# Optimization experiments

Hardware: AMD Instinct MI355X
Metric: run time of the kernel (lower is better)

## Reference

```python
import jax, jax.numpy as jnp
import numpy as np

B, N, C_IN, C_OUT, NUM_TYPES = 4, 4096, 128, 64, 5
TEMP = 1.0  # self.temp is undefined in the source; use 1.0


def setup_inputs() -> dict:
    key = jax.random.key(0)
    ks = jax.random.split(key, 9)
    bound_p = np.sqrt(6.0 / (C_IN + C_OUT))
    bound_k = np.sqrt(6.0 / (C_OUT + 1))
    return {
        "node_rep": jax.random.normal(ks[0], (B, N, C_IN), dtype=jnp.float32),
        "adj_matrix": jax.random.uniform(ks[1], (N, N), dtype=jnp.float32),
        "node_type": jax.random.randint(ks[2], (N,), 0, NUM_TYPES),
        "proj_W": jax.random.uniform(ks[3], (C_OUT, C_IN), minval=-bound_p, maxval=bound_p, dtype=jnp.float32),
        "proj_b": jnp.zeros((C_OUT,), dtype=jnp.float32),
        "k_W": jax.random.uniform(ks[4], (NUM_TYPES, C_OUT), minval=-bound_k, maxval=bound_k, dtype=jnp.float32),
        "k_b": jnp.zeros((NUM_TYPES,), dtype=jnp.float32),
        "v_W": jax.random.uniform(ks[5], (NUM_TYPES, C_OUT), minval=-bound_k, maxval=bound_k, dtype=jnp.float32),
        "v_b": jnp.zeros((NUM_TYPES,), dtype=jnp.float32),
    }


def reference(node_rep, adj_matrix, node_type, proj_W, proj_b, k_W, k_b, v_W, v_b):
    # projection: [B,N,c_in] -> [B,N,c_out]
    h = jnp.einsum('bnc,oc->bno', node_rep, proj_W) + proj_b
    # per-type scalar scores stacked: [B,N,num_types]
    ks = jnp.einsum('bno,to->bnt', h, k_W) + k_b
    vs = jnp.einsum('bno,to->bnt', h, v_W) + v_b
    # gather score of each node's own type -> [B,N,1]
    idx = jnp.broadcast_to(node_type[None, :, None], (h.shape[0], h.shape[1], 1))
    f1 = jnp.take_along_axis(ks, idx, axis=2)           # [B,N,1]
    f2 = jnp.take_along_axis(vs, idx, axis=2)           # [B,N,1]
    # pairwise logits masked/weighted by adjacency: [B,N,N]
    attn_logits = adj_matrix[None, :, :] * (f1 + jnp.swapaxes(f2, 1, 2))
    unnorm = jax.nn.sigmoid(attn_logits) - 0.5
    attn_probs = jax.nn.softmax(unnorm / TEMP, axis=1)  # softmax over dim 1, as in source
    # aggregate: [B,N,N] @ [B,N,c_out] -> [B,N,c_out]
    return jnp.matmul(attn_probs, h)
```

## Files before the change

### kernel.cpp

```cpp
#include <hip/hip_runtime.h>
#include <hip/hip_bf16.h>
#include <stdint.h>

#define NN   4096
#define BB   4
#define CIN  128
#define COUT 64

typedef __attribute__((ext_vector_type(4))) float f32x4;
typedef __attribute__((ext_vector_type(8))) short s16x8;
typedef __attribute__((ext_vector_type(4))) int   i32x4;

__device__ __forceinline__ float sig_exp(float u) {
    const float L = 1.4426950408889634f;
    float e0 = __builtin_amdgcn_exp2f(-u * L);
    float sg = __builtin_amdgcn_rcpf(1.0f + e0);
    return __builtin_amdgcn_exp2f(__builtin_fmaf(sg, L, -0.7213475204444817f));
}

__device__ __forceinline__ short f2bf(float x) {
    unsigned u = __builtin_bit_cast(unsigned, x);
    return (short)((u + 0x8000u) >> 16);
}

__global__ void k_zero(float* __restrict__ p, int n) {
    int i = blockIdx.x * blockDim.x + threadIdx.x;
    if (i < n) p[i] = 0.0f;
}

__global__ __launch_bounds__(256) void k_proj(
    const float* __restrict__ node_rep, const int* __restrict__ node_type,
    const float* __restrict__ pW, const float* __restrict__ pb,
    const float* __restrict__ kW, const float* __restrict__ kb,
    const float* __restrict__ vW, const float* __restrict__ vb,
    float* __restrict__ h, float* __restrict__ f1, float* __restrict__ f2)
{
    int row = blockIdx.x * 4 + (threadIdx.x >> 6);
    int o   = threadIdx.x & 63;
    int n   = row & (NN - 1);

    const f32x4* xr = (const f32x4*)(node_rep + (size_t)row * CIN);
    const f32x4* wr = (const f32x4*)(pW + (size_t)o * CIN);
    float acc = pb[o];
    #pragma unroll
    for (int c = 0; c < CIN / 4; ++c) {
        f32x4 x = xr[c], w = wr[c];
        acc = fmaf(x[0], w[0], acc);
        acc = fmaf(x[1], w[1], acc);
        acc = fmaf(x[2], w[2], acc);
        acc = fmaf(x[3], w[3], acc);
    }
    h[(size_t)row * COUT + o] = acc;

    int t = node_type[n];
    float s1 = acc * kW[t * COUT + o];
    float s2 = acc * vW[t * COUT + o];
    #pragma unroll
    for (int off = 32; off; off >>= 1) {
        s1 += __shfl_xor(s1, off, 64);
        s2 += __shfl_xor(s2, off, 64);
    }
    if (o == 0) { f1[row] = s1 + kb[t]; f2[row] = s2 + vb[t]; }
}

__global__ __launch_bounds__(256) void k_denom(
    const float* __restrict__ adj, const float* __restrict__ f1,
    const float* __restrict__ f2, float* __restrict__ denom)
{
    int j  = blockIdx.x * 256 + threadIdx.x;
    int i0 = blockIdx.y * 128;
    float f2r[BB], acc[BB];
    #pragma unroll
    for (int b = 0; b < BB; ++b) { f2r[b] = f2[b * NN + j]; acc[b] = 0.0f; }
    for (int ii = 0; ii < 128; ++ii) {
        int i = i0 + ii;
        float a = adj[(size_t)i * NN + j];
        #pragma unroll
        for (int b = 0; b < BB; ++b) {
            float u = a * (f1[b * NN + i] + f2r[b]);
            acc[b] += sig_exp(u);
        }
    }
    #pragma unroll
    for (int b = 0; b < BB; ++b) atomicAdd(&denom[b * NN + j], acc[b]);
}

__global__ __launch_bounds__(256) void k_hst(
    const float* __restrict__ h, const float* __restrict__ denom,
    unsigned short* __restrict__ hsT)
{
    int b  = blockIdx.y;
    int j0 = blockIdx.x * 64;
    __shared__ float tile[64][65];
    int cx = threadIdx.x & 63;
    int ry = threadIdx.x >> 6;
    #pragma unroll
    for (int k = 0; k < 16; ++k) {
        int jl = k * 4 + ry;
        float d = denom[b * NN + j0 + jl];
        tile[jl][cx] = h[((size_t)b * NN + j0 + jl) * COUT + cx] / d;
    }
    __syncthreads();
    #pragma unroll
    for (int k = 0; k < 16; ++k) {
        int cl = k * 4 + ry;
        hsT[((size_t)b * COUT + cl) * NN + j0 + cx] = (unsigned short)f2bf(tile[cx][cl]);
    }
}

__global__ __launch_bounds__(512) void k_out(
    const float* __restrict__ adj, const float* __restrict__ f1,
    const float* __restrict__ f2, const unsigned short* __restrict__ hsT,
    float* __restrict__ out)
{
    int i0   = blockIdx.x * 16;
    int tid  = threadIdx.x;
    int wid  = tid >> 6;
    int lane = tid & 63;
    int lrow = lane & 15;
    int lgrp = lane >> 4;

    const float* arow = adj + (size_t)(i0 + lrow) * NN;
    float f1v[BB];
    #pragma unroll
    for (int b = 0; b < BB; ++b) f1v[b] = f1[b * NN + i0 + lrow];

    f32x4 acc[BB][4];
    #pragma unroll
    for (int b = 0; b < BB; ++b)
        #pragma unroll
        for (int r = 0; r < 4; ++r) acc[b][r] = (f32x4){0.f, 0.f, 0.f, 0.f};

    int jbeg = wid * (NN / 8);
    for (int js = 0; js < NN / 8; js += 32) {
        int jk = jbeg + js + lgrp * 8;
        f32x4 a0 = *(const f32x4*)(arow + jk);
        f32x4 a1 = *(const f32x4*)(arow + jk + 4);

        #pragma unroll
        for (int b = 0; b < BB; ++b) {
            const float* f2b = f2 + b * NN;
            f32x4 s0 = *(const f32x4*)(f2b + jk);
            f32x4 s1 = *(const f32x4*)(f2b + jk + 4);

            float e[8];
            #pragma unroll
            for (int q = 0; q < 4; ++q) {
                e[q]     = sig_exp(a0[q] * (f1v[b] + s0[q]));
                e[q + 4] = sig_exp(a1[q] * (f1v[b] + s1[q]));
            }
            s16x8 af;
            #pragma unroll
            for (int q = 0; q < 8; ++q) af[q] = f2bf(e[q]);

            const unsigned short* hsb = hsT + (size_t)b * COUT * NN;
            s16x8 b0 = __builtin_bit_cast(s16x8, *(const i32x4*)(hsb + (size_t)(0  + lrow) * NN + jk));
            s16x8 b1 = __builtin_bit_cast(s16x8, *(const i32x4*)(hsb + (size_t)(16 + lrow) * NN + jk));
            s16x8 b2 = __builtin_bit_cast(s16x8, *(const i32x4*)(hsb + (size_t)(32 + lrow) * NN + jk));
            s16x8 b3 = __builtin_bit_cast(s16x8, *(const i32x4*)(hsb + (size_t)(48 + lrow) * NN + jk));

            acc[b][0] = __builtin_amdgcn_mfma_f32_16x16x32_bf16(af, b0, acc[b][0], 0, 0, 0);
            acc[b][1] = __builtin_amdgcn_mfma_f32_16x16x32_bf16(af, b1, acc[b][1], 0, 0, 0);
            acc[b][2] = __builtin_amdgcn_mfma_f32_16x16x32_bf16(af, b2, acc[b][2], 0, 0, 0);
            acc[b][3] = __builtin_amdgcn_mfma_f32_16x16x32_bf16(af, b3, acc[b][3], 0, 0, 0);
        }
    }

    __shared__ float red[8][16][64];
    #pragma unroll
    for (int b = 0; b < BB; ++b) {
        if (b) __syncthreads();
        #pragma unroll
        for (int r = 0; r < 4; ++r) {
            red[wid][lgrp * 4 + r][ 0 + lrow] = acc[b][0][r];
            red[wid][lgrp * 4 + r][16 + lrow] = acc[b][1][r];
            red[wid][lgrp * 4 + r][32 + lrow] = acc[b][2][r];
            red[wid][lgrp * 4 + r][48 + lrow] = acc[b][3][r];
        }
        __syncthreads();

        int e2 = tid * 2;
        int ii = e2 >> 6;
        int cc = e2 & 63;
        float sx = 0.f, sy = 0.f;
        #pragma unroll
        for (int w = 0; w < 8; ++w) {
            sx += red[w][ii][cc];
            sy += red[w][ii][cc + 1];
        }
        float* op = out + ((size_t)b * NN + i0 + ii) * COUT + cc;
        op[0] = sx; op[1] = sy;
    }
}

extern "C" void kernel_launch(void* const* d_in, const int* in_sizes, int n_in,
                              void* d_out, int out_size, void* d_ws, size_t ws_size,
                              hipStream_t stream)
{
    const float* node_rep = (const float*)d_in[0];
    const float* adj      = (const float*)d_in[1];
    const int*   ntype    = (const int*)  d_in[2];
    const float* pW       = (const float*)d_in[3];
    const float* pb       = (const float*)d_in[4];
    const float* kW       = (const float*)d_in[5];
    const float* kb       = (const float*)d_in[6];
    const float* vW       = (const float*)d_in[7];
    const float* vb       = (const float*)d_in[8];
    float* out = (float*)d_out;

    char* w = (char*)d_ws;
    float*          h     = (float*)(w);
    float*          f1    = (float*)(w + 4194304);
    float*          f2    = (float*)(w + 4259840);
    float*          denom = (float*)(w + 4325376);
    unsigned short* hsT   = (unsigned short*)(w + 4390912);

    k_zero <<<64, 256, 0, stream>>>(denom, BB * NN);
    k_proj <<<BB * NN / 4, 256, 0, stream>>>(node_rep, ntype, pW, pb, kW, kb, vW, vb, h, f1, f2);
    k_denom<<<dim3(NN / 256, 32), 256, 0, stream>>>(adj, f1, f2, denom);
    k_hst  <<<dim3(NN / 64, BB), 256, 0, stream>>>(h, denom, hsT);
    k_out  <<<dim3(NN / 16), 512, 0, stream>>>(adj, f1, f2, hsT, out);
}
```

Measured before the change: 334.0 us.

## Split denominator and output reductions into partial buffers with separate reduce kernels

The column-sum kernel now uses finer row tiles, so there are more blocks. It writes per-tile partial sums to a workspace, and a new reduce kernel turns them into reciprocal denominators. This replaces the atomics and the zeroing kernel. The output kernel splits the j dimension into four grid slices so more blocks are in flight, and a new kernel adds up the four partial outputs. The projection also uses four independent accumulators. The cost is extra workspace traffic, two extra launches, and a partial buffer of 16 MB for the output.

```diff
diff --git a/kernel.cpp b/kernel.cpp
--- a/kernel.cpp
+++ b/kernel.cpp
@@ -6,6 +6,9 @@
 #define BB   4
 #define CIN  128
 #define COUT 64
+#define JSPL 4
+#define ITIL 32
+#define NIT  (NN / ITIL)
 
 typedef __attribute__((ext_vector_type(4))) float f32x4;
 typedef __attribute__((ext_vector_type(8))) short s16x8;
@@ -21,11 +24,6 @@
 __device__ __forceinline__ short f2bf(float x) {
     unsigned u = __builtin_bit_cast(unsigned, x);
     return (short)((u + 0x8000u) >> 16);
-}
-
-__global__ void k_zero(float* __restrict__ p, int n) {
-    int i = blockIdx.x * blockDim.x + threadIdx.x;
-    if (i < n) p[i] = 0.0f;
 }
 
 __global__ __launch_bounds__(256) void k_proj(
@@ -41,15 +39,16 @@
 
     const f32x4* xr = (const f32x4*)(node_rep + (size_t)row * CIN);
     const f32x4* wr = (const f32x4*)(pW + (size_t)o * CIN);
-    float acc = pb[o];
+    float a0 = pb[o], a1 = 0.f, a2 = 0.f, a3 = 0.f;
     #pragma unroll
     for (int c = 0; c < CIN / 4; ++c) {
         f32x4 x = xr[c], w = wr[c];
-        acc = fmaf(x[0], w[0], acc);
-        acc = fmaf(x[1], w[1], acc);
-        acc = fmaf(x[2], w[2], acc);
-        acc = fmaf(x[3], w[3], acc);
-    }
+        a0 = fmaf(x[0], w[0], a0);
+        a1 = fmaf(x[1], w[1], a1);
+        a2 = fmaf(x[2], w[2], a2);
+        a3 = fmaf(x[3], w[3], a3);
+    }
+    float acc = (a0 + a1) + (a2 + a3);
     h[(size_t)row * COUT + o] = acc;
 
     int t = node_type[n];
@@ -65,28 +64,40 @@
 
 __global__ __launch_bounds__(256) void k_denom(
     const float* __restrict__ adj, const float* __restrict__ f1,
-    const float* __restrict__ f2, float* __restrict__ denom)
+    const float* __restrict__ f2, float* __restrict__ pd)
 {
     int j  = blockIdx.x * 256 + threadIdx.x;
-    int i0 = blockIdx.y * 128;
+    int it = blockIdx.y;
+    int i0 = it * ITIL;
     float f2r[BB], acc[BB];
     #pragma unroll
     for (int b = 0; b < BB; ++b) { f2r[b] = f2[b * NN + j]; acc[b] = 0.0f; }
-    for (int ii = 0; ii < 128; ++ii) {
-        int i = i0 + ii;
-        float a = adj[(size_t)i * NN + j];
+    #pragma unroll 2
+    for (int ii = 0; ii < ITIL; ii += 2) {
+        float a0 = adj[(size_t)(i0 + ii)     * NN + j];
+        float a1 = adj[(size_t)(i0 + ii + 1) * NN + j];
         #pragma unroll
         for (int b = 0; b < BB; ++b) {
-            float u = a * (f1[b * NN + i] + f2r[b]);
-            acc[b] += sig_exp(u);
-        }
-    }
-    #pragma unroll
-    for (int b = 0; b < BB; ++b) atomicAdd(&denom[b * NN + j], acc[b]);
+            float fa = f1[b * NN + i0 + ii];
+            float fb = f1[b * NN + i0 + ii + 1];
+            acc[b] += sig_exp(a0 * (fa + f2r[b])) + sig_exp(a1 * (fb + f2r[b]));
+        }
+    }
+    #pragma unroll
+    for (int b = 0; b < BB; ++b) pd[(size_t)(it * BB + b) * NN + j] = acc[b];
+}
+
+__global__ __launch_bounds__(256) void k_dred(
+    const float* __restrict__ pd, float* __restrict__ rden)
+{
+    int gid = blockIdx.x * 256 + threadIdx.x;
+    float s = 0.0f;
+    for (int it = 0; it < NIT; ++it) s += pd[(size_t)it * BB * NN + gid];
+    rden[gid] = 1.0f / s;
 }
 
 __global__ __launch_bounds__(256) void k_hst(
-    const float* __restrict__ h, const float* __restrict__ denom,
+    const float* __restrict__ h, const float* __restrict__ rden,
     unsigned short* __restrict__ hsT)
 {
     int b  = blockIdx.y;
@@ -97,8 +108,8 @@
     #pragma unroll
     for (int k = 0; k < 16; ++k) {
         int jl = k * 4 + ry;
-        float d = denom[b * NN + j0 + jl];
-        tile[jl][cx] = h[((size_t)b * NN + j0 + jl) * COUT + cx] / d;
+        float d = rden[b * NN + j0 + jl];
+        tile[jl][cx] = h[((size_t)b * NN + j0 + jl) * COUT + cx] * d;
     }
     __syncthreads();
     #pragma unroll
@@ -111,9 +122,10 @@
 __global__ __launch_bounds__(512) void k_out(
     const float* __restrict__ adj, const float* __restrict__ f1,
     const float* __restrict__ f2, const unsigned short* __restrict__ hsT,
-    float* __restrict__ out)
+    float* __restrict__ pout)
 {
     int i0   = blockIdx.x * 16;
+    int jsp  = blockIdx.y;
     int tid  = threadIdx.x;
     int wid  = tid >> 6;
     int lane = tid & 63;
@@ -131,8 +143,8 @@
         #pragma unroll
         for (int r = 0; r < 4; ++r) acc[b][r] = (f32x4){0.f, 0.f, 0.f, 0.f};
 
-    int jbeg = wid * (NN / 8);
-    for (int js = 0; js < NN / 8; js += 32) {
+    int jbeg = jsp * (NN / JSPL) + wid * (NN / JSPL / 8);
+    for (int js = 0; js < NN / JSPL / 8; js += 32) {
         int jk = jbeg + js + lgrp * 8;
         f32x4 a0 = *(const f32x4*)(arow + jk);
         f32x4 a1 = *(const f32x4*)(arow + jk + 4);
@@ -188,9 +200,20 @@
             sx += red[w][ii][cc];
             sy += red[w][ii][cc + 1];
         }
-        float* op = out + ((size_t)b * NN + i0 + ii) * COUT + cc;
+        float* op = pout + ((size_t)(jsp * BB + b) * NN + i0 + ii) * COUT + cc;
         op[0] = sx; op[1] = sy;
     }
+}
+
+__global__ __launch_bounds__(256) void k_ored(
+    const float* __restrict__ pout, float* __restrict__ out)
+{
+    size_t e = ((size_t)blockIdx.x * 256 + threadIdx.x) * 4;
+    f32x4 s = *(const f32x4*)(pout + e);
+    #pragma unroll
+    for (int sp = 1; sp < JSPL; ++sp)
+        s += *(const f32x4*)(pout + (size_t)sp * BB * NN * COUT + e);
+    *(f32x4*)(out + e) = s;
 }
 
 extern "C" void kernel_launch(void* const* d_in, const int* in_sizes, int n_in,
@@ -212,12 +235,15 @@
     float*          h     = (float*)(w);
     float*          f1    = (float*)(w + 4194304);
     float*          f2    = (float*)(w + 4259840);
-    float*          denom = (float*)(w + 4325376);
+    float*          rden  = (float*)(w + 4325376);
     unsigned short* hsT   = (unsigned short*)(w + 4390912);
-
-    k_zero <<<64, 256, 0, stream>>>(denom, BB * NN);
+    float*          pd    = (float*)(w + 6488064);
+    float*          pout  = (float*)(w + 14876672);
+
     k_proj <<<BB * NN / 4, 256, 0, stream>>>(node_rep, ntype, pW, pb, kW, kb, vW, vb, h, f1, f2);
-    k_denom<<<dim3(NN / 256, 32), 256, 0, stream>>>(adj, f1, f2, denom);
-    k_hst  <<<dim3(NN / 64, BB), 256, 0, stream>>>(h, denom, hsT);
-    k_out  <<<dim3(NN / 16), 512, 0, stream>>>(adj, f1, f2, hsT, out);
-}
+    k_denom<<<dim3(NN / 256, NIT), 256, 0, stream>>>(adj, f1, f2, pd);
+    k_dred <<<BB * NN / 256, 256, 0, stream>>>(pd, rden);
+    k_hst  <<<dim3(NN / 64, BB), 256, 0, stream>>>(h, rden, hsT);
+    k_out  <<<dim3(NN / 16, JSPL), 512, 0, stream>>>(adj, f1, f2, hsT, pout);
+    k_ored <<<BB * NN * COUT / 1024, 256, 0, stream>>>(pout, out);
+}
```

After: 286.6 us. 1.17x faster.
